# Kernel tuning notes

Hardware: AMD Instinct MI355X
Metric: run time of the kernel (lower is better)

Reference implementation:

```python
import jax, jax.numpy as jnp
import numpy as np

B, S, D = 2, 512, 2048
INNER = 512
H = 16
DH = D // H
FFN = 8192
SLOTS = 32
EPS = 1e-6


def rmsnorm(x, w):
    # norm = ||x|| / sqrt(D); out = w * x / (norm + eps)   (matches torch RMSNorm above)
    norm = jnp.linalg.norm(x, axis=-1, keepdims=True) / np.sqrt(x.shape[-1])
    return w * x / (norm + EPS)


def setup_inputs() -> dict:
    key = jax.random.key(0)
    ks = jax.random.split(key, 32)
    s = 0.02
    def lin(k, din, dout):
        k1, k2 = jax.random.split(k)
        return (jax.random.normal(k1, (din, dout), jnp.float32) * s,
                jnp.zeros((dout,), jnp.float32))
    Wq, bq = lin(ks[0], D, D)
    Wk, bk = lin(ks[1], D, D)
    Wv, bv = lin(ks[2], D, D)
    Wz, bz = lin(ks[3], D, D)
    Wg, bg = lin(ks[4], D, D)
    Wd1, bd1 = lin(ks[5], D, INNER)   # MDI context-modulated decay bottleneck
    Wd2, bd2 = lin(ks[6], INNER, D)
    Wmi, _ = lin(ks[7], D, D)         # MDI integration (input)
    Wmh, bm = lin(ks[8], D, D)        # MDI integration (hidden)
    Wo, bo = lin(ks[9], D, D)         # multi-memory attention output proj
    W1f, b1f = lin(ks[10], D, FFN)
    W2f, b2f = lin(ks[11], FFN, D)
    x = jax.random.normal(ks[12], (B, S, D), jnp.float32)
    return dict(x=x, Wq=Wq, bq=bq, Wk=Wk, bk=bk, Wv=Wv, bv=bv, Wz=Wz, bz=bz,
                Wg=Wg, bg=bg, n1w=jnp.ones((D,), jnp.float32), n2w=jnp.ones((D,), jnp.float32),
                Wd1=Wd1, bd1=bd1, Wd2=Wd2, bd2=bd2, Wmi=Wmi, Wmh=Wmh, bm=bm,
                Wo=Wo, bo=bo, W1f=W1f, b1f=b1f, W2f=W2f, b2f=b2f)


def _forward(x, Wq, bq, Wk, bk, Wv, bv, Wz, bz, Wg, bg, n1w, n2w,
             Wd1, bd1, Wd2, bd2, Wmi, Wmh, bm, Wo, bo, W1f, b1f, W2f, b2f):
    b, s, d = x.shape
    # Kernel fusion: precompute QKVZ for the whole sequence (as in use_kernel_fusion=True)
    xn = rmsnorm(x, n1w)
    q = xn @ Wq + bq
    k = xn @ Wk + bk
    v = xn @ Wv + bv
    z = xn @ Wz + bz

    scale = 1.0 / np.sqrt(DH)

    def step(carry, inp):
        h_prev, bank, t = carry            # h_prev:[b,d], bank:[b,SLOTS,d]
        x_t, q_t, k_t, v_t, z_t = inp      # each [b,d]
        # MDI: context-modulated decay gamma in (0,1), integrated candidate h_new
        gamma = jax.nn.sigmoid(jax.nn.relu(k_t @ Wd1 + bd1) @ Wd2 + bd2)
        h_new = jnp.tanh(z_t @ Wmi + h_prev @ Wmh + bm)
        # Core formula: h_t = z_t * sigma(W_g h_{t-1}) + gamma * h_{t-1} (+0.1*h_new)
        gate = jax.nn.sigmoid(h_prev @ Wg + bg)
        h_t = z_t * gate + gamma * h_prev + 0.1 * h_new
        # Multi-memory attention over memory bank (K=V=stored h states)
        qh = q_t.reshape(b, H, DH)
        kh = bank.reshape(b, SLOTS, H, DH)
        scores = jnp.einsum('bhd,bshd->bhs', qh, kh) * scale
        attn = jax.nn.softmax(scores, axis=-1)
        ctx = jnp.einsum('bhs,bshd->bhd', attn, kh).reshape(b, d)
        mem_ctx = ctx @ Wo + bo
        h_att = h_t + mem_ctx + 0.1 * v_t
        x_res = x_t + h_att                # dropout is identity in eval
        # sequential state update: write h_t into circular slot
        bank = bank.at[:, t % SLOTS].set(h_t)
        return (h_t, bank, t + 1), x_res

    h0 = jnp.zeros((b, d), x.dtype)
    bank0 = jnp.zeros((b, SLOTS, d), x.dtype)
    xs = tuple(jnp.swapaxes(a, 0, 1) for a in (x, q, k, v, z))  # [s,b,d]
    _, x_res_seq = jax.lax.scan(step, (h0, bank0, jnp.int32(0)), xs)
    x_res = jnp.swapaxes(x_res_seq, 0, 1)  # [b,s,d]
    # FFN + residual (vectorized over the whole sequence)
    ffn_out = jax.nn.gelu(rmsnorm(x_res, n2w) @ W1f + b1f, approximate=False) @ W2f + b2f
    return x_res + ffn_out


def reference(x, Wq, bq, Wk, bk, Wv, bv, Wz, bz, Wg, bg, n1w, n2w,
              Wd1, bd1, Wd2, bd2, Wmi, Wmh, bm, Wo, bo, W1f, b1f, W2f, b2f):
    return _forward(x, Wq, bq, Wk, bk, Wv, bv, Wz, bz, Wg, bg, n1w, n2w,
                    Wd1, bd1, Wd2, bd2, Wmi, Wmh, bm, Wo, bo, W1f, b1f, W2f, b2f)
```

## Files before the change

### kernel.cpp

```cpp
#include <hip/hip_runtime.h>

typedef unsigned short u16;
typedef unsigned int   u32;
typedef __attribute__((ext_vector_type(8))) short  short8;
typedef __attribute__((ext_vector_type(4))) float  f32x4;

#define D_     2048
#define S_     512
#define B_     2
#define FFN_   8192
#define INNER_ 512
#define NROW   1024
#define SNBLK  256
#define SNGRP  16
#define SGRPSZ 16
#define CPAD   32

__device__ u16 g_WqT[D_*D_], g_WkT[D_*D_], g_WvT[D_*D_], g_WzT[D_*D_];
__device__ u16 g_WgT[D_*D_], g_WmhT[D_*D_], g_WmiT[D_*D_], g_WoT[D_*D_];
__device__ u16 g_Wd1T[INNER_*D_], g_Wd2T[D_*INNER_];
__device__ u16 g_W1fT[FFN_*D_], g_W2fT[D_*FFN_];
__device__ u16 g_xn[NROW*D_], g_q[NROW*D_], g_k[NROW*D_], g_v[NROW*D_], g_z[NROW*D_];
__device__ u16 g_t1[NROW*INNER_];
__device__ float g_gamma[NROW*D_], g_zWmi[NROW*D_], g_H[NROW*D_];
__device__ float g_memctx[NROW*D_], g_xres[NROW*D_];
__device__ u16 g_ctx[NROW*D_], g_xrn[NROW*D_], g_ffn1[NROW*FFN_];
__device__ u32 g_cnt[SNGRP * CPAD];
__device__ u32 g_root[CPAD];
__device__ u32 g_gen[CPAD];

__device__ __forceinline__ float b2f(u16 u) {
  union { u32 i; float f; } c; c.i = ((u32)u) << 16; return c.f;
}
__device__ __forceinline__ u16 f2b(float f) {
  union { float f; u32 i; } c; c.f = f;
  u32 u = c.i;
  return (u16)((u + 0x7fffu + ((u >> 16) & 1u)) >> 16);
}

__global__ __launch_bounds__(256) void transpose_k(const float* __restrict__ in,
                                                   u16* __restrict__ out,
                                                   int K, int N) {
  __shared__ u16 tl[64][72];
  int kb = blockIdx.x * 64, nb = blockIdx.y * 64;
  {
    int rh = threadIdx.x >> 4;
    int c4 = (threadIdx.x & 15) * 4;
#pragma unroll
    for (int rr = 0; rr < 64; rr += 16) {
      int r = rr + rh;
      float4 v4 = *(const float4*)&in[(size_t)(kb + r) * N + nb + c4];
      tl[r][c4]     = f2b(v4.x);
      tl[r][c4 + 1] = f2b(v4.y);
      tl[r][c4 + 2] = f2b(v4.z);
      tl[r][c4 + 3] = f2b(v4.w);
    }
  }
  __syncthreads();
  {
    int rh = threadIdx.x >> 3;
    int c8 = (threadIdx.x & 7) * 8;
#pragma unroll
    for (int rr = 0; rr < 64; rr += 32) {
      int n = rr + rh;
      u16 tmp[8];
#pragma unroll
      for (int i = 0; i < 8; ++i) tmp[i] = tl[c8 + i][n];
      *(uint4*)&out[(size_t)(nb + n) * K + kb + c8] = *(const uint4*)tmp;
    }
  }
}

__global__ __launch_bounds__(256) void rmsnorm_k(const float* __restrict__ x,
                                                 const float* __restrict__ w,
                                                 u16* __restrict__ out) {
  __shared__ float red[4];
  int row = blockIdx.x;
  const float* xr = x + (size_t)row * D_;
  int base = threadIdx.x * 8;
  float4 a = *(const float4*)&xr[base];
  float4 b = *(const float4*)&xr[base + 4];
  float xs[8] = {a.x, a.y, a.z, a.w, b.x, b.y, b.z, b.w};
  float s = 0.f;
#pragma unroll
  for (int i = 0; i < 8; ++i) s += xs[i] * xs[i];
  for (int off = 32; off >= 1; off >>= 1) s += __shfl_xor(s, off);
  int wave = threadIdx.x >> 6;
  if ((threadIdx.x & 63) == 0) red[wave] = s;
  __syncthreads();
  float tot = red[0] + red[1] + red[2] + red[3];
  float sc = 1.f / (sqrtf(tot * (1.f / (float)D_)) + 1e-6f);
  float4 wa = *(const float4*)&w[base];
  float4 wb = *(const float4*)&w[base + 4];
  float ws[8] = {wa.x, wa.y, wa.z, wa.w, wb.x, wb.y, wb.z, wb.w};
  u32 po[4];
#pragma unroll
  for (int i = 0; i < 4; ++i)
    po[i] = (u32)f2b(xs[2*i] * sc * ws[2*i]) | ((u32)f2b(xs[2*i+1] * sc * ws[2*i+1]) << 16);
  *(uint4*)&out[(size_t)row * D_ + base] = *(const uint4*)po;
}

template <int EPI>
__global__ __launch_bounds__(256, 2)
void gemm_bt(const u16* __restrict__ A, const u16* __restrict__ BT,
             const float* __restrict__ bias, const float* __restrict__ res,
             void* __restrict__ outp, int M, int N, int K) {
  __shared__ u16 As[128 * 40];
  __shared__ u16 Bs[128 * 40];
  const int tid = threadIdx.x;
  const int wave = tid >> 6, lane = tid & 63;
  const int m0 = blockIdx.x * 128, n0 = blockIdx.y * 128;
  const int ar = tid >> 2;
  const int ac = (tid & 3) * 8;
  const u16* Ag = A + (size_t)(m0 + ar) * K + ac;
  const u16* Bg = BT + (size_t)(n0 + ar) * K + ac;
  uint4 pa0 = *(const uint4*)Ag;
  uint4 pa1 = *(const uint4*)(Ag + (size_t)64 * K);
  uint4 pb0 = *(const uint4*)Bg;
  uint4 pb1 = *(const uint4*)(Bg + (size_t)64 * K);
  const int wm = (wave >> 1) * 64, wn = (wave & 1) * 64;
  const int q = lane >> 4, mr = lane & 15;
  const int q8 = q * 8;
  f32x4 acc[4][4];
#pragma unroll
  for (int mi = 0; mi < 4; ++mi)
#pragma unroll
    for (int ni = 0; ni < 4; ++ni) { acc[mi][ni][0]=0.f; acc[mi][ni][1]=0.f; acc[mi][ni][2]=0.f; acc[mi][ni][3]=0.f; }

  for (int k0 = 0; k0 < K; k0 += 32) {
    __syncthreads();
    *(uint4*)&As[ar * 40 + ac] = pa0;
    *(uint4*)&As[(ar + 64) * 40 + ac] = pa1;
    *(uint4*)&Bs[ar * 40 + ac] = pb0;
    *(uint4*)&Bs[(ar + 64) * 40 + ac] = pb1;
    __syncthreads();
    if (k0 + 32 < K) {
      pa0 = *(const uint4*)(Ag + k0 + 32);
      pa1 = *(const uint4*)(Ag + (size_t)64 * K + k0 + 32);
      pb0 = *(const uint4*)(Bg + k0 + 32);
      pb1 = *(const uint4*)(Bg + (size_t)64 * K + k0 + 32);
    }
    short8 af[4], bv[4];
#pragma unroll
    for (int mi = 0; mi < 4; ++mi) af[mi] = *(const short8*)&As[(wm + mi * 16 + mr) * 40 + q8];
#pragma unroll
    for (int ni = 0; ni < 4; ++ni) bv[ni] = *(const short8*)&Bs[(wn + ni * 16 + mr) * 40 + q8];
#pragma unroll
    for (int mi = 0; mi < 4; ++mi)
#pragma unroll
      for (int ni = 0; ni < 4; ++ni)
        acc[mi][ni] = __builtin_amdgcn_mfma_f32_16x16x32_bf16(af[mi], bv[ni], acc[mi][ni], 0, 0, 0);
  }
  float* outf = (float*)outp;
  u16* outh = (u16*)outp;
#pragma unroll
  for (int mi = 0; mi < 4; ++mi)
#pragma unroll
    for (int r = 0; r < 4; ++r) {
      int row = m0 + wm + mi * 16 + q * 4 + r;
#pragma unroll
      for (int ni = 0; ni < 4; ++ni) {
        int col = n0 + wn + ni * 16 + mr;
        float v = acc[mi][ni][r];
        if (bias) v += bias[col];
        if (EPI == 1) v = fmaxf(v, 0.f);
        if (EPI == 2) v = 1.f / (1.f + __expf(-v));
        if (EPI == 3) v = 0.5f * v * (1.f + erff(v * 0.70710678118654752f));
        if (EPI == 5) v += res[(size_t)row * N + col];
        if (EPI == 2 || EPI == 4 || EPI == 5) outf[(size_t)row * N + col] = v;
        else                                  outh[(size_t)row * N + col] = f2b(v);
      }
    }
}

__device__ __forceinline__ void grid_barrier() {
  __syncthreads();
  if (threadIdx.x == 0) {
    u32 g0 = __hip_atomic_load(&g_gen[0], __ATOMIC_RELAXED, __HIP_MEMORY_SCOPE_AGENT);
    asm volatile("" ::: "memory");
    int grp = blockIdx.x & (SNGRP - 1);
    u32 n = __hip_atomic_fetch_add(&g_cnt[grp * CPAD], 1u, __ATOMIC_RELAXED, __HIP_MEMORY_SCOPE_AGENT);
    bool done = false;
    if (n == SGRPSZ - 1) {
      u32 r = __hip_atomic_fetch_add(&g_root[0], 1u, __ATOMIC_RELAXED, __HIP_MEMORY_SCOPE_AGENT);
      if (r == SNGRP - 1) {
        for (int i = 0; i < SNGRP; ++i)
          __hip_atomic_store(&g_cnt[i * CPAD], 0u, __ATOMIC_RELAXED, __HIP_MEMORY_SCOPE_AGENT);
        __hip_atomic_store(&g_root[0], 0u, __ATOMIC_RELAXED, __HIP_MEMORY_SCOPE_AGENT);
        asm volatile("s_waitcnt vmcnt(0)" ::: "memory");
        __hip_atomic_fetch_add(&g_gen[0], 1u, __ATOMIC_RELAXED, __HIP_MEMORY_SCOPE_AGENT);
        done = true;
      }
    }
    if (!done) {
      while (__hip_atomic_load(&g_gen[0], __ATOMIC_RELAXED, __HIP_MEMORY_SCOPE_AGENT) == g0)
        __builtin_amdgcn_s_sleep(1);
    }
    asm volatile("" ::: "memory");
  }
  __syncthreads();
}

__global__ __launch_bounds__(256, 1)
void scan_kernel(const u16* __restrict__ WgT, const u16* __restrict__ WmhT,
                 const u16* __restrict__ zb, const float* __restrict__ gammab,
                 const float* __restrict__ zWmib, const float* __restrict__ bg,
                 const float* __restrict__ bm, float* __restrict__ Hst) {
  __shared__ float he[D_ / 2];
  __shared__ float ho[D_ / 2];
  __shared__ float dotbuf[32];
  const int tid = threadIdx.x, wave = tid >> 6, lane = tid & 63;
  const int b = blockIdx.x >> 7;
  const int j0 = (blockIdx.x & 127) * 16;

  u32 w_reg[8][16];
#pragma unroll
  for (int c = 0; c < 8; ++c) {
    int cc = wave * 8 + c;
    const u16* Wt = (cc < 16 ? WgT : WmhT) + (size_t)(j0 + (cc & 15)) * D_;
#pragma unroll
    for (int i = 0; i < 16; ++i)
      w_reg[c][i] = *(const u32*)&Wt[i * 128 + lane * 2];
  }
  for (int i = tid; i < D_ / 2; i += 256) { he[i] = 0.f; ho[i] = 0.f; }

  const int jj = tid;
  float pbg = 0.f, pbm = 0.f;
  if (tid < 16) { pbg = bg[j0 + jj]; pbm = bm[j0 + jj]; }
  __syncthreads();

  for (int t = 0; t < S_; ++t) {
    size_t off = ((size_t)b * S_ + t) * D_ + j0 + jj;
    float pz = 0.f, pg = 0.f, pzw = 0.f;
    if (tid < 16) { pz = b2f(zb[off]); pg = gammab[off]; pzw = zWmib[off]; }

    float acc[8];
#pragma unroll
    for (int c = 0; c < 8; ++c) acc[c] = 0.f;
#pragma unroll
    for (int i = 0; i < 16; ++i) {
      float hx = he[i * 64 + lane];
      float hy = ho[i * 64 + lane];
#pragma unroll
      for (int c = 0; c < 8; ++c) {
        u32 w = w_reg[c][i];
        float w0 = b2f((u16)(w & 0xffff));
        float w1 = b2f((u16)(w >> 16));
        acc[c] += w0 * hx + w1 * hy;
      }
    }
#pragma unroll
    for (int c = 0; c < 8; ++c) {
      float v = acc[c];
      for (int o = 32; o >= 1; o >>= 1) v += __shfl_xor(v, o);
      if (lane == 0) dotbuf[wave * 8 + c] = v;
    }
    __syncthreads();
    if (tid < 16) {
      int j = j0 + jj;
      float gd = dotbuf[jj] + pbg;
      float md = dotbuf[16 + jj] + pbm;
      float gate = 1.f / (1.f + __expf(-gd));
      float hnew = tanhf(pzw + md);
      float hprev = (j & 1) ? ho[j >> 1] : he[j >> 1];
      float hv = pz * gate + pg * hprev + 0.1f * hnew;
      __hip_atomic_store(&Hst[off], hv, __ATOMIC_RELAXED, __HIP_MEMORY_SCOPE_AGENT);
    }
    asm volatile("s_waitcnt vmcnt(0)" ::: "memory");
    grid_barrier();
    {
      float* src = (float*)&Hst[((size_t)b * S_ + t) * D_];
      int base = tid * 8;
      float v[8];
#pragma unroll
      for (int u = 0; u < 8; ++u)
        v[u] = __hip_atomic_load(&src[base + u], __ATOMIC_RELAXED, __HIP_MEMORY_SCOPE_AGENT);
      int p = base >> 1;
      he[p] = v[0]; he[p + 1] = v[2]; he[p + 2] = v[4]; he[p + 3] = v[6];
      ho[p] = v[1]; ho[p + 1] = v[3]; ho[p + 2] = v[5]; ho[p + 3] = v[7];
    }
    __syncthreads();
  }
}

__global__ __launch_bounds__(256)
void attn_kernel(const u16* __restrict__ Q, const float* __restrict__ Hst,
                 u16* __restrict__ CTX) {
  __shared__ float qs[4][128];
  const int wave = threadIdx.x >> 6, lane = threadIdx.x & 63;
  const int task = blockIdx.x * 4 + wave;
  const int h = task & 15;
  const int t = (task >> 4) & (S_ - 1);
  const int b = task >> 13;
  const int row = b * S_ + t;
  {
    u32 qv = *(const u32*)&Q[(size_t)row * D_ + h * 128 + lane * 2];
    qs[wave][lane * 2]     = b2f((u16)(qv & 0xffff));
    qs[wave][lane * 2 + 1] = b2f((u16)(qv >> 16));
  }
  __syncthreads();
  const int s = lane & 31, half = lane >> 5;
  int j = t - 1 - s;
  bool valid = (t > 0) && (j >= 0);
  float dot = 0.f;
  if (valid) {
    const float* Krow = Hst + ((size_t)b * S_ + j) * D_ + h * 128 + half * 64;
    const float* qp = &qs[wave][half * 64];
#pragma unroll
    for (int it = 0; it < 16; ++it) {
      float4 kv = *(const float4*)&Krow[it * 4];
      dot += qp[it*4] * kv.x + qp[it*4+1] * kv.y + qp[it*4+2] * kv.z + qp[it*4+3] * kv.w;
    }
  }
  dot += __shfl_xor(dot, 32);
  float score = valid ? dot * 0.08838834764831843f : 0.f;
  float mx = score;
  for (int off = 16; off >= 1; off >>= 1) mx = fmaxf(mx, __shfl_xor(mx, off));
  float p = __expf(score - mx);
  float sum = p;
  for (int off = 16; off >= 1; off >>= 1) sum += __shfl_xor(sum, off);
  float aw = p / sum;
  float cx = 0.f, cy = 0.f;
  for (int ss = 0; ss < 32; ++ss) {
    float a = __shfl(aw, ss);
    int jj2 = t - 1 - ss;
    if (t > 0 && jj2 >= 0) {
      float2 kv = *(const float2*)&Hst[((size_t)b * S_ + jj2) * D_ + h * 128 + lane * 2];
      cx += a * kv.x; cy += a * kv.y;
    }
  }
  u32 o = (u32)f2b(cx) | ((u32)f2b(cy) << 16);
  *(u32*)&CTX[(size_t)row * D_ + h * 128 + lane * 2] = o;
}

__global__ __launch_bounds__(256)
void combine_k(const float* __restrict__ x, const u16* __restrict__ v,
               const float* __restrict__ Hs, const float* __restrict__ mc,
               float* __restrict__ xres) {
  size_t i = ((size_t)blockIdx.x * 256 + threadIdx.x) * 4;
  float4 xv = *(const float4*)&x[i];
  uint2 vv = *(const uint2*)&v[i];
  float4 hh = *(const float4*)&Hs[i];
  float4 m  = *(const float4*)&mc[i];
  float4 o;
  o.x = xv.x + hh.x + m.x + 0.1f * b2f((u16)(vv.x & 0xffff));
  o.y = xv.y + hh.y + m.y + 0.1f * b2f((u16)(vv.x >> 16));
  o.z = xv.z + hh.z + m.z + 0.1f * b2f((u16)(vv.y & 0xffff));
  o.w = xv.w + hh.w + m.w + 0.1f * b2f((u16)(vv.y >> 16));
  *(float4*)&xres[i] = o;
}

static void* sym(const void* s) { void* p = nullptr; (void)hipGetSymbolAddress(&p, s); return p; }

extern "C" void kernel_launch(void* const* d_in, const int* in_sizes, int n_in,
                              void* d_out, int out_size, void* d_ws, size_t ws_size,
                              hipStream_t stream) {
  (void)in_sizes; (void)n_in; (void)d_ws; (void)ws_size; (void)out_size;
  const float* x   = (const float*)d_in[0];
  const float* Wq  = (const float*)d_in[1];  const float* bq  = (const float*)d_in[2];
  const float* Wk  = (const float*)d_in[3];  const float* bk  = (const float*)d_in[4];
  const float* Wv  = (const float*)d_in[5];  const float* bv  = (const float*)d_in[6];
  const float* Wz  = (const float*)d_in[7];  const float* bz  = (const float*)d_in[8];
  const float* Wg  = (const float*)d_in[9];  const float* bg  = (const float*)d_in[10];
  const float* n1w = (const float*)d_in[11]; const float* n2w = (const float*)d_in[12];
  const float* Wd1 = (const float*)d_in[13]; const float* bd1 = (const float*)d_in[14];
  const float* Wd2 = (const float*)d_in[15]; const float* bd2 = (const float*)d_in[16];
  const float* Wmi = (const float*)d_in[17];
  const float* Wmh = (const float*)d_in[18]; const float* bm  = (const float*)d_in[19];
  const float* Wo  = (const float*)d_in[20]; const float* bo  = (const float*)d_in[21];
  const float* W1f = (const float*)d_in[22]; const float* b1f = (const float*)d_in[23];
  const float* W2f = (const float*)d_in[24]; const float* b2f_ = (const float*)d_in[25];

  u16* WqT  = (u16*)sym(HIP_SYMBOL(g_WqT));   u16* WkT  = (u16*)sym(HIP_SYMBOL(g_WkT));
  u16* WvT  = (u16*)sym(HIP_SYMBOL(g_WvT));   u16* WzT  = (u16*)sym(HIP_SYMBOL(g_WzT));
  u16* WgT  = (u16*)sym(HIP_SYMBOL(g_WgT));   u16* WmhT = (u16*)sym(HIP_SYMBOL(g_WmhT));
  u16* WmiT = (u16*)sym(HIP_SYMBOL(g_WmiT));  u16* WoT  = (u16*)sym(HIP_SYMBOL(g_WoT));
  u16* Wd1T = (u16*)sym(HIP_SYMBOL(g_Wd1T));  u16* Wd2T = (u16*)sym(HIP_SYMBOL(g_Wd2T));
  u16* W1fT = (u16*)sym(HIP_SYMBOL(g_W1fT));  u16* W2fT = (u16*)sym(HIP_SYMBOL(g_W2fT));
  u16* xn  = (u16*)sym(HIP_SYMBOL(g_xn));
  u16* qb  = (u16*)sym(HIP_SYMBOL(g_q));   u16* kb2 = (u16*)sym(HIP_SYMBOL(g_k));
  u16* vb  = (u16*)sym(HIP_SYMBOL(g_v));   u16* zb  = (u16*)sym(HIP_SYMBOL(g_z));
  u16* t1  = (u16*)sym(HIP_SYMBOL(g_t1));
  float* gamma  = (float*)sym(HIP_SYMBOL(g_gamma));
  float* zWmi   = (float*)sym(HIP_SYMBOL(g_zWmi));
  float* Hst    = (float*)sym(HIP_SYMBOL(g_H));
  float* memctx = (float*)sym(HIP_SYMBOL(g_memctx));
  float* xres   = (float*)sym(HIP_SYMBOL(g_xres));
  u16* ctx  = (u16*)sym(HIP_SYMBOL(g_ctx));
  u16* xrn  = (u16*)sym(HIP_SYMBOL(g_xrn));
  u16* ffn1 = (u16*)sym(HIP_SYMBOL(g_ffn1));

  transpose_k<<<dim3(32, 32), 256, 0, stream>>>(Wq,  WqT,  D_, D_);
  transpose_k<<<dim3(32, 32), 256, 0, stream>>>(Wk,  WkT,  D_, D_);
  transpose_k<<<dim3(32, 32), 256, 0, stream>>>(Wv,  WvT,  D_, D_);
  transpose_k<<<dim3(32, 32), 256, 0, stream>>>(Wz,  WzT,  D_, D_);
  transpose_k<<<dim3(32, 32), 256, 0, stream>>>(Wg,  WgT,  D_, D_);
  transpose_k<<<dim3(32, 32), 256, 0, stream>>>(Wmh, WmhT, D_, D_);
  transpose_k<<<dim3(32, 32), 256, 0, stream>>>(Wmi, WmiT, D_, D_);
  transpose_k<<<dim3(32, 32), 256, 0, stream>>>(Wo,  WoT,  D_, D_);
  transpose_k<<<dim3(32, 8),  256, 0, stream>>>(Wd1, Wd1T, D_, INNER_);
  transpose_k<<<dim3(8, 32),  256, 0, stream>>>(Wd2, Wd2T, INNER_, D_);
  transpose_k<<<dim3(32, 128), 256, 0, stream>>>(W1f, W1fT, D_, FFN_);
  transpose_k<<<dim3(128, 32), 256, 0, stream>>>(W2f, W2fT, FFN_, D_);

  rmsnorm_k<<<NROW, 256, 0, stream>>>(x, n1w, xn);

  gemm_bt<0><<<dim3(8, 16), 256, 0, stream>>>(xn, WqT, bq, nullptr, qb,  NROW, D_, D_);
  gemm_bt<0><<<dim3(8, 16), 256, 0, stream>>>(xn, WkT, bk, nullptr, kb2, NROW, D_, D_);
  gemm_bt<0><<<dim3(8, 16), 256, 0, stream>>>(xn, WvT, bv, nullptr, vb,  NROW, D_, D_);
  gemm_bt<0><<<dim3(8, 16), 256, 0, stream>>>(xn, WzT, bz, nullptr, zb,  NROW, D_, D_);

  gemm_bt<1><<<dim3(8, 4),  256, 0, stream>>>(kb2, Wd1T, bd1, nullptr, t1,    NROW, INNER_, D_);
  gemm_bt<2><<<dim3(8, 16), 256, 0, stream>>>(t1,  Wd2T, bd2, nullptr, gamma, NROW, D_, INNER_);
  gemm_bt<4><<<dim3(8, 16), 256, 0, stream>>>(zb,  WmiT, nullptr, nullptr, zWmi, NROW, D_, D_);

  scan_kernel<<<SNBLK, 256, 0, stream>>>(WgT, WmhT, zb, gamma, zWmi, bg, bm, Hst);

  attn_kernel<<<4096, 256, 0, stream>>>(qb, Hst, ctx);
  gemm_bt<4><<<dim3(8, 16), 256, 0, stream>>>(ctx, WoT, bo, nullptr, memctx, NROW, D_, D_);
  combine_k<<<2048, 256, 0, stream>>>(x, vb, Hst, memctx, xres);

  rmsnorm_k<<<NROW, 256, 0, stream>>>(xres, n2w, xrn);
  gemm_bt<3><<<dim3(8, 64), 256, 0, stream>>>(xrn,  W1fT, b1f, nullptr, ffn1, NROW, FFN_, D_);
  gemm_bt<5><<<dim3(8, 16), 256, 0, stream>>>(ffn1, W2fT, b2f_, xres, (float*)d_out, NROW, D_, FFN_);
}
```

Measured before the change: 4.423 ms.

## Use per-step per-batch barriers and fp16 dot2 in recurrent scan kernel

Replaces the global grid barrier in the scan kernel with per-timestep, per-batch hierarchical counters, so each batch's 128 blocks synchronize only among themselves and no reset or generation phase is needed. The counters are zeroed by memsets before launch. Hidden state is now kept in shared memory as packed fp16 and the Wg/Wmh weights in registers as fp16, so the matvec uses fdot2 instead of unpacking bf16 to fp32. The previous h value is read back from global memory. Converting the state and weights to fp16 adds rounding error on the recurrent path.

```diff
diff --git a/kernel.cpp b/kernel.cpp
--- a/kernel.cpp
+++ b/kernel.cpp
@@ -4,6 +4,7 @@
 typedef unsigned int   u32;
 typedef __attribute__((ext_vector_type(8))) short  short8;
 typedef __attribute__((ext_vector_type(4))) float  f32x4;
+typedef __attribute__((ext_vector_type(2))) _Float16 half2_t;
 
 #define D_     2048
 #define S_     512
@@ -12,9 +13,6 @@
 #define INNER_ 512
 #define NROW   1024
 #define SNBLK  256
-#define SNGRP  16
-#define SGRPSZ 16
-#define CPAD   32
 
 __device__ u16 g_WqT[D_*D_], g_WkT[D_*D_], g_WvT[D_*D_], g_WzT[D_*D_];
 __device__ u16 g_WgT[D_*D_], g_WmhT[D_*D_], g_WmiT[D_*D_], g_WoT[D_*D_];
@@ -25,9 +23,8 @@
 __device__ float g_gamma[NROW*D_], g_zWmi[NROW*D_], g_H[NROW*D_];
 __device__ float g_memctx[NROW*D_], g_xres[NROW*D_];
 __device__ u16 g_ctx[NROW*D_], g_xrn[NROW*D_], g_ffn1[NROW*FFN_];
-__device__ u32 g_cnt[SNGRP * CPAD];
-__device__ u32 g_root[CPAD];
-__device__ u32 g_gen[CPAD];
+__device__ u32 g_agrp[S_ * 2 * 16 * 16];
+__device__ u32 g_aroot[S_ * 2 * 16];
 
 __device__ __forceinline__ float b2f(u16 u) {
   union { u32 i; float f; } c; c.i = ((u32)u) << 16; return c.f;
@@ -173,81 +170,58 @@
     }
 }
 
-__device__ __forceinline__ void grid_barrier() {
-  __syncthreads();
-  if (threadIdx.x == 0) {
-    u32 g0 = __hip_atomic_load(&g_gen[0], __ATOMIC_RELAXED, __HIP_MEMORY_SCOPE_AGENT);
-    asm volatile("" ::: "memory");
-    int grp = blockIdx.x & (SNGRP - 1);
-    u32 n = __hip_atomic_fetch_add(&g_cnt[grp * CPAD], 1u, __ATOMIC_RELAXED, __HIP_MEMORY_SCOPE_AGENT);
-    bool done = false;
-    if (n == SGRPSZ - 1) {
-      u32 r = __hip_atomic_fetch_add(&g_root[0], 1u, __ATOMIC_RELAXED, __HIP_MEMORY_SCOPE_AGENT);
-      if (r == SNGRP - 1) {
-        for (int i = 0; i < SNGRP; ++i)
-          __hip_atomic_store(&g_cnt[i * CPAD], 0u, __ATOMIC_RELAXED, __HIP_MEMORY_SCOPE_AGENT);
-        __hip_atomic_store(&g_root[0], 0u, __ATOMIC_RELAXED, __HIP_MEMORY_SCOPE_AGENT);
-        asm volatile("s_waitcnt vmcnt(0)" ::: "memory");
-        __hip_atomic_fetch_add(&g_gen[0], 1u, __ATOMIC_RELAXED, __HIP_MEMORY_SCOPE_AGENT);
-        done = true;
-      }
-    }
-    if (!done) {
-      while (__hip_atomic_load(&g_gen[0], __ATOMIC_RELAXED, __HIP_MEMORY_SCOPE_AGENT) == g0)
-        __builtin_amdgcn_s_sleep(1);
-    }
-    asm volatile("" ::: "memory");
-  }
-  __syncthreads();
-}
-
 __global__ __launch_bounds__(256, 1)
 void scan_kernel(const u16* __restrict__ WgT, const u16* __restrict__ WmhT,
                  const u16* __restrict__ zb, const float* __restrict__ gammab,
                  const float* __restrict__ zWmib, const float* __restrict__ bg,
                  const float* __restrict__ bm, float* __restrict__ Hst) {
-  __shared__ float he[D_ / 2];
-  __shared__ float ho[D_ / 2];
+  __shared__ half2_t hpk[D_ / 2];
   __shared__ float dotbuf[32];
   const int tid = threadIdx.x, wave = tid >> 6, lane = tid & 63;
   const int b = blockIdx.x >> 7;
-  const int j0 = (blockIdx.x & 127) * 16;
-
-  u32 w_reg[8][16];
+  const int blk = blockIdx.x & 127;
+  const int j0 = blk * 16;
+  const int grp = blk >> 3;
+
+  half2_t w_reg[8][16];
 #pragma unroll
   for (int c = 0; c < 8; ++c) {
     int cc = wave * 8 + c;
     const u16* Wt = (cc < 16 ? WgT : WmhT) + (size_t)(j0 + (cc & 15)) * D_;
 #pragma unroll
-    for (int i = 0; i < 16; ++i)
-      w_reg[c][i] = *(const u32*)&Wt[i * 128 + lane * 2];
-  }
-  for (int i = tid; i < D_ / 2; i += 256) { he[i] = 0.f; ho[i] = 0.f; }
-
-  const int jj = tid;
+    for (int i = 0; i < 16; ++i) {
+      u32 w = *(const u32*)&Wt[i * 128 + lane * 2];
+      half2_t p;
+      p[0] = (_Float16)b2f((u16)(w & 0xffff));
+      p[1] = (_Float16)b2f((u16)(w >> 16));
+      w_reg[c][i] = p;
+    }
+  }
+  {
+    half2_t zz; zz[0] = (_Float16)0.f; zz[1] = (_Float16)0.f;
+    for (int i = tid; i < D_ / 2; i += 256) hpk[i] = zz;
+  }
   float pbg = 0.f, pbm = 0.f;
-  if (tid < 16) { pbg = bg[j0 + jj]; pbm = bm[j0 + jj]; }
+  if (tid < 16) { pbg = bg[j0 + tid]; pbm = bm[j0 + tid]; }
   __syncthreads();
 
   for (int t = 0; t < S_; ++t) {
-    size_t off = ((size_t)b * S_ + t) * D_ + j0 + jj;
-    float pz = 0.f, pg = 0.f, pzw = 0.f;
-    if (tid < 16) { pz = b2f(zb[off]); pg = gammab[off]; pzw = zWmib[off]; }
+    size_t off = ((size_t)b * S_ + t) * D_ + j0 + tid;
+    float pz = 0.f, pg = 0.f, pzw = 0.f, php = 0.f;
+    if (tid < 16) {
+      pz = b2f(zb[off]); pg = gammab[off]; pzw = zWmib[off];
+      if (t > 0) php = __hip_atomic_load(&Hst[off - D_], __ATOMIC_RELAXED, __HIP_MEMORY_SCOPE_AGENT);
+    }
 
     float acc[8];
 #pragma unroll
     for (int c = 0; c < 8; ++c) acc[c] = 0.f;
 #pragma unroll
     for (int i = 0; i < 16; ++i) {
-      float hx = he[i * 64 + lane];
-      float hy = ho[i * 64 + lane];
-#pragma unroll
-      for (int c = 0; c < 8; ++c) {
-        u32 w = w_reg[c][i];
-        float w0 = b2f((u16)(w & 0xffff));
-        float w1 = b2f((u16)(w >> 16));
-        acc[c] += w0 * hx + w1 * hy;
-      }
+      half2_t h2 = hpk[i * 64 + lane];
+#pragma unroll
+      for (int c = 0; c < 8; ++c)
+        acc[c] = __builtin_amdgcn_fdot2(w_reg[c][i], h2, acc[c], false);
     }
 #pragma unroll
     for (int c = 0; c < 8; ++c) {
@@ -257,27 +231,43 @@
     }
     __syncthreads();
     if (tid < 16) {
-      int j = j0 + jj;
-      float gd = dotbuf[jj] + pbg;
-      float md = dotbuf[16 + jj] + pbm;
+      float gd = dotbuf[tid] + pbg;
+      float md = dotbuf[16 + tid] + pbm;
       float gate = 1.f / (1.f + __expf(-gd));
       float hnew = tanhf(pzw + md);
-      float hprev = (j & 1) ? ho[j >> 1] : he[j >> 1];
-      float hv = pz * gate + pg * hprev + 0.1f * hnew;
+      float hv = pz * gate + pg * php + 0.1f * hnew;
       __hip_atomic_store(&Hst[off], hv, __ATOMIC_RELAXED, __HIP_MEMORY_SCOPE_AGENT);
     }
-    asm volatile("s_waitcnt vmcnt(0)" ::: "memory");
-    grid_barrier();
+    if (tid == 0) {
+      asm volatile("s_waitcnt vmcnt(0)" ::: "memory");
+      u32* gc = &g_agrp[(((size_t)t * 2 + b) * 16 + grp) * 16];
+      u32* rt = &g_aroot[((size_t)t * 2 + b) * 16];
+      u32 n = __hip_atomic_fetch_add(gc, 1u, __ATOMIC_RELAXED, __HIP_MEMORY_SCOPE_AGENT);
+      bool done = false;
+      if (n == 7) {
+        u32 r = __hip_atomic_fetch_add(rt, 1u, __ATOMIC_RELAXED, __HIP_MEMORY_SCOPE_AGENT);
+        if (r == 15) done = true;
+      }
+      if (!done) {
+        while (__hip_atomic_load(rt, __ATOMIC_RELAXED, __HIP_MEMORY_SCOPE_AGENT) < 16u)
+          __builtin_amdgcn_s_sleep(1);
+      }
+    }
+    __syncthreads();
     {
-      float* src = (float*)&Hst[((size_t)b * S_ + t) * D_];
+      const float* src = &Hst[((size_t)b * S_ + t) * D_];
       int base = tid * 8;
       float v[8];
 #pragma unroll
       for (int u = 0; u < 8; ++u)
         v[u] = __hip_atomic_load(&src[base + u], __ATOMIC_RELAXED, __HIP_MEMORY_SCOPE_AGENT);
-      int p = base >> 1;
-      he[p] = v[0]; he[p + 1] = v[2]; he[p + 2] = v[4]; he[p + 3] = v[6];
-      ho[p] = v[1]; ho[p + 1] = v[3]; ho[p + 2] = v[5]; ho[p + 3] = v[7];
+      half2_t p0, p1, p2, p3;
+      p0[0] = (_Float16)v[0]; p0[1] = (_Float16)v[1];
+      p1[0] = (_Float16)v[2]; p1[1] = (_Float16)v[3];
+      p2[0] = (_Float16)v[4]; p2[1] = (_Float16)v[5];
+      p3[0] = (_Float16)v[6]; p3[1] = (_Float16)v[7];
+      int p = tid * 4;
+      hpk[p] = p0; hpk[p + 1] = p1; hpk[p + 2] = p2; hpk[p + 3] = p3;
     }
     __syncthreads();
   }
@@ -389,6 +379,11 @@
   u16* ctx  = (u16*)sym(HIP_SYMBOL(g_ctx));
   u16* xrn  = (u16*)sym(HIP_SYMBOL(g_xrn));
   u16* ffn1 = (u16*)sym(HIP_SYMBOL(g_ffn1));
+  void* agrp  = sym(HIP_SYMBOL(g_agrp));
+  void* aroot = sym(HIP_SYMBOL(g_aroot));
+
+  hipMemsetAsync(agrp,  0, (size_t)S_ * 2 * 16 * 16 * 4, stream);
+  hipMemsetAsync(aroot, 0, (size_t)S_ * 2 * 16 * 4, stream);
 
   transpose_k<<<dim3(32, 32), 256, 0, stream>>>(Wq,  WqT,  D_, D_);
   transpose_k<<<dim3(32, 32), 256, 0, stream>>>(Wk,  WkT,  D_, D_);
```

New measurement: 4.438 ms. No clear change (+0.3%).
